# Optimization experiments

Hardware: AMD Instinct MI355X
Metric: run time of the kernel (lower is better)

The kernel has to match this reference:

```python
import jax, jax.numpy as jnp
import numpy as np

# ShiftedSteSign forward: binary sign (0 -> +1). STE only matters for backward.

def ste_sign(x):
    return jnp.where(x >= 0, 1.0, -1.0).astype(x.dtype)

N, D, U, E = 32768, 1024, 1024, 3  # tokens, d_in, units, kernel_estimators


def setup_inputs() -> dict:
    key = jax.random.key(0)
    kx, k0, k1, k2 = jax.random.split(key, 4)
    x = jax.random.normal(kx, (N, D), dtype=jnp.float32)
    # keras 'random_uniform' initializer default range [-0.05, 0.05]
    kernels = [jax.random.uniform(k, (D, U), jnp.float32, -0.05, 0.05) for k in (k0, k1, k2)]
    # alpha initialized as ||kernel||_1 along axis 0 divided by d_in (trainable)
    alphas = [jnp.sum(jnp.abs(kw), axis=0) / D for kw in kernels]
    return {"x": x,
            "k0": kernels[0], "k1": kernels[1], "k2": kernels[2],
            "a0": alphas[0], "a1": alphas[1], "a2": alphas[2]}


def reference(x, k0, k1, k2, a0, a1, a2):
    d = x.shape[-1]
    xq = ste_sign(x)                                   # [N, D] binary
    beta = jnp.sum(jnp.abs(x), axis=-1) / d            # [N]
    out = jnp.zeros((x.shape[0], k0.shape[1]), x.dtype)
    for kw, a in ((k0, a0), (k1, a1), (k2, a2)):
        Z = xq @ ste_sign(kw)                          # binary GEMM [N, U]
        out = out + Z * (beta[:, None] * a[None, :])   # outer-product scale
    return out
```

## Files before the change

kernel.cpp:

```cpp
#include <hip/hip_runtime.h>
#include <hip/hip_bf16.h>
#include <stdint.h>

#define N_TOK 32768
#define D_IN  1024
#define U_OUT 1024

typedef __attribute__((ext_vector_type(4))) int int32x4;

__device__ __forceinline__ void async_copy16(const void* g, void* l) {
  __builtin_amdgcn_global_load_lds(
      (const __attribute__((address_space(1))) void*)g,
      (__attribute__((address_space(3))) void*)l,
      16, 0, 0);
}

__global__ __launch_bounds__(256) void quant_kernel(
    const float* __restrict__ x,
    char* __restrict__ xq,
    float* __restrict__ beta) {
  const int wave = threadIdx.x >> 6;
  const int lane = threadIdx.x & 63;
  const int row  = blockIdx.x * 4 + wave;

  const float4* p = (const float4*)(x + (size_t)row * D_IN);
  alignas(16) char sb[16];
  float asum = 0.f;
  #pragma unroll
  for (int j = 0; j < 4; ++j) {
    const float4 v = p[lane * 4 + j];
    asum += fabsf(v.x) + fabsf(v.y) + fabsf(v.z) + fabsf(v.w);
    sb[j * 4 + 0] = (v.x >= 0.f) ? 1 : -1;
    sb[j * 4 + 1] = (v.y >= 0.f) ? 1 : -1;
    sb[j * 4 + 2] = (v.z >= 0.f) ? 1 : -1;
    sb[j * 4 + 3] = (v.w >= 0.f) ? 1 : -1;
  }
  *(int32x4*)(xq + (size_t)row * D_IN + lane * 16) = *(const int32x4*)sb;

  #pragma unroll
  for (int off = 32; off > 0; off >>= 1)
    asum += __shfl_down(asum, off, 64);
  if (lane == 0) beta[row] = asum * (1.0f / (float)D_IN);
}

__global__ __launch_bounds__(256) void wt_kernel(
    const float* __restrict__ k0, const float* __restrict__ k1,
    const float* __restrict__ k2,
    const float* __restrict__ a0, const float* __restrict__ a1,
    const float* __restrict__ a2,
    char* __restrict__ wt,
    float* __restrict__ q) {
  const int tid = threadIdx.x;
  const int d0  = blockIdx.x * 16;
  const int u0  = tid * 4;

  const float4 av0 = *(const float4*)(a0 + u0);
  const float4 av1 = *(const float4*)(a1 + u0);
  const float4 av2 = *(const float4*)(a2 + u0);
  float4 s;
  s.x = fmaxf(av0.x + av1.x + av2.x, 1e-20f);
  s.y = fmaxf(av0.y + av1.y + av2.y, 1e-20f);
  s.z = fmaxf(av0.z + av1.z + av2.z, 1e-20f);
  s.w = fmaxf(av0.w + av1.w + av2.w, 1e-20f);
  if (blockIdx.x == 0) {
    float4 qv;
    qv.x = s.x * (1.0f / 127.0f); qv.y = s.y * (1.0f / 127.0f);
    qv.z = s.z * (1.0f / 127.0f); qv.w = s.w * (1.0f / 127.0f);
    *(float4*)(q + u0) = qv;
  }
  const float4 inv = {127.0f / s.x, 127.0f / s.y, 127.0f / s.z, 127.0f / s.w};

  alignas(16) char buf[4][16];
  #pragma unroll
  for (int d = 0; d < 16; ++d) {
    const size_t off = (size_t)(d0 + d) * U_OUT + u0;
    const float4 v0 = *(const float4*)(k0 + off);
    const float4 v1 = *(const float4*)(k1 + off);
    const float4 v2 = *(const float4*)(k2 + off);
    float4 w;
    w.x = (v0.x >= 0.f ? av0.x : -av0.x) + (v1.x >= 0.f ? av1.x : -av1.x)
        + (v2.x >= 0.f ? av2.x : -av2.x);
    w.y = (v0.y >= 0.f ? av0.y : -av0.y) + (v1.y >= 0.f ? av1.y : -av1.y)
        + (v2.y >= 0.f ? av2.y : -av2.y);
    w.z = (v0.z >= 0.f ? av0.z : -av0.z) + (v1.z >= 0.f ? av1.z : -av1.z)
        + (v2.z >= 0.f ? av2.z : -av2.z);
    w.w = (v0.w >= 0.f ? av0.w : -av0.w) + (v1.w >= 0.f ? av1.w : -av1.w)
        + (v2.w >= 0.f ? av2.w : -av2.w);
    buf[0][d] = (char)(int)rintf(w.x * inv.x);
    buf[1][d] = (char)(int)rintf(w.y * inv.y);
    buf[2][d] = (char)(int)rintf(w.z * inv.z);
    buf[3][d] = (char)(int)rintf(w.w * inv.w);
  }
  #pragma unroll
  for (int j = 0; j < 4; ++j)
    *(int32x4*)(wt + (size_t)(u0 + j) * D_IN + d0) = *(const int32x4*)buf[j];
}

#define BM 128
#define BN 128
#define BK 64

__global__ __launch_bounds__(256, 2) void gemm_kernel(
    const char* __restrict__ A,
    const char* __restrict__ Bt,
    const float* __restrict__ beta,
    const float* __restrict__ q,
    float* __restrict__ C) {
  const int K = D_IN, N = U_OUT;
  __shared__ char As[BM * BK];
  __shared__ char Bs[BN * BK];

  const int bid = blockIdx.x;
  const int xcd = bid & 7;
  const int g   = bid >> 3;
  const int mt  = xcd * 32 + (g >> 3);
  const int nt  = g & 7;
  const int m0  = mt * BM;
  const int n0  = nt * BN;

  const int tid  = threadIdx.x;
  const int wave = tid >> 6;
  const int lane = tid & 63;
  const int wr   = wave >> 1;
  const int wc   = wave & 1;
  const int lrow = lane & 15;
  const int quad = lane >> 4;

  int32x4 acc[4][4] = {};

  for (int kk = 0; kk < K; kk += BK) {
    #pragma unroll
    for (int half = 0; half < 2; half++) {
      const int s   = tid + half * 256;
      const int row = s >> 2;
      const int c   = (s & 3) * 16;
      async_copy16(A  + (size_t)(m0 + row) * K + kk + c, As + (size_t)s * 16);
      async_copy16(Bt + (size_t)(n0 + row) * K + kk + c, Bs + (size_t)s * 16);
    }
    __syncthreads();

    int32x4 af[4], bf[4];
    #pragma unroll
    for (int i = 0; i < 4; i++) {
      af[i] = *(const int32x4*)(As + (wr * 64 + i * 16 + lrow) * BK + quad * 16);
      bf[i] = *(const int32x4*)(Bs + (wc * 64 + i * 16 + lrow) * BK + quad * 16);
    }
    #pragma unroll
    for (int mi = 0; mi < 4; mi++)
      #pragma unroll
      for (int ni = 0; ni < 4; ni++)
        acc[mi][ni] = __builtin_amdgcn_mfma_i32_16x16x64_i8(
            af[mi], bf[ni], acc[mi][ni], 0, 0, 0);
    __syncthreads();
  }

  #pragma unroll
  for (int mi = 0; mi < 4; mi++) {
    #pragma unroll
    for (int r = 0; r < 4; r++) {
      const int row = m0 + wr * 64 + mi * 16 + quad * 4 + r;
      const float b = beta[row];
      #pragma unroll
      for (int ni = 0; ni < 4; ni++) {
        const int col = n0 + wc * 64 + ni * 16 + lrow;
        C[(size_t)row * N + col] = (float)acc[mi][ni][r] * b * q[col];
      }
    }
  }
}

extern "C" void kernel_launch(void* const* d_in, const int* in_sizes, int n_in,
                              void* d_out, int out_size, void* d_ws, size_t ws_size,
                              hipStream_t stream) {
  const float* x  = (const float*)d_in[0];
  const float* k0 = (const float*)d_in[1];
  const float* k1 = (const float*)d_in[2];
  const float* k2 = (const float*)d_in[3];
  const float* a0 = (const float*)d_in[4];
  const float* a1 = (const float*)d_in[5];
  const float* a2 = (const float*)d_in[6];
  float* out = (float*)d_out;

  char* ws = (char*)d_ws;
  char*  xq   = ws;
  char*  wt   = ws + (size_t)N_TOK * D_IN;
  float* q    = (float*)(wt + (size_t)U_OUT * D_IN);
  float* beta = q + U_OUT;

  quant_kernel<<<N_TOK / 4, 256, 0, stream>>>(x, xq, beta);
  wt_kernel<<<64, 256, 0, stream>>>(k0, k1, k2, a0, a1, a2, wt, q);
  gemm_kernel<<<(N_TOK / BM) * (U_OUT / BN), 256, 0, stream>>>(xq, wt, beta, q, out);
}
```

Before: 289.7 us.

## Pipeline int8 GEMM with triple-buffered LDS, bigger tiles, and swizzled layout

The GEMM moves from 128x128 tiles with 256 threads to 256x256 tiles with 512 threads. A three-stage LDS ring prefetches the next K tiles with global_load_lds while MFMAs run, and an XOR swizzle is added to cut LDS bank conflicts. Each K step is split into two MFMA phases with barriers and s_setprio, q is hoisted into registers for the epilogue, and the quantize kernel switches to coalesced 4-byte stores. The costs are higher LDS and register use per block and hand-tuned vmcnt waits that must line up with the prefetch order.

Result: no change. 294.0 us (+1.5%).

```diff
diff --git a/kernel.cpp b/kernel.cpp
--- a/kernel.cpp
+++ b/kernel.cpp
@@ -1,5 +1,4 @@
 #include <hip/hip_runtime.h>
-#include <hip/hip_bf16.h>
 #include <stdint.h>
 
 #define N_TOK 32768
@@ -24,19 +23,18 @@
   const int row  = blockIdx.x * 4 + wave;
 
   const float4* p = (const float4*)(x + (size_t)row * D_IN);
-  alignas(16) char sb[16];
+  uint32_t* outw = (uint32_t*)(xq + (size_t)row * D_IN);
   float asum = 0.f;
   #pragma unroll
   for (int j = 0; j < 4; ++j) {
-    const float4 v = p[lane * 4 + j];
+    const float4 v = p[j * 64 + lane];
     asum += fabsf(v.x) + fabsf(v.y) + fabsf(v.z) + fabsf(v.w);
-    sb[j * 4 + 0] = (v.x >= 0.f) ? 1 : -1;
-    sb[j * 4 + 1] = (v.y >= 0.f) ? 1 : -1;
-    sb[j * 4 + 2] = (v.z >= 0.f) ? 1 : -1;
-    sb[j * 4 + 3] = (v.w >= 0.f) ? 1 : -1;
-  }
-  *(int32x4*)(xq + (size_t)row * D_IN + lane * 16) = *(const int32x4*)sb;
-
+    uint32_t w =  (uint32_t)(uint8_t)(char)(v.x >= 0.f ? 1 : -1)
+               | ((uint32_t)(uint8_t)(char)(v.y >= 0.f ? 1 : -1) << 8)
+               | ((uint32_t)(uint8_t)(char)(v.z >= 0.f ? 1 : -1) << 16)
+               | ((uint32_t)(uint8_t)(char)(v.w >= 0.f ? 1 : -1) << 24);
+    outw[j * 64 + lane] = w;
+  }
   #pragma unroll
   for (int off = 32; off > 0; off >>= 1)
     asum += __shfl_down(asum, off, 64);
@@ -96,74 +94,128 @@
     *(int32x4*)(wt + (size_t)(u0 + j) * D_IN + d0) = *(const int32x4*)buf[j];
 }
 
-#define BM 128
-#define BN 128
-#define BK 64
-
-__global__ __launch_bounds__(256, 2) void gemm_kernel(
+#define BM 256
+#define BN 256
+#define BKT 64
+#define NKT (D_IN / BKT)
+
+__global__ __launch_bounds__(512, 2) void gemm_kernel(
     const char* __restrict__ A,
     const char* __restrict__ Bt,
     const float* __restrict__ beta,
     const float* __restrict__ q,
     float* __restrict__ C) {
-  const int K = D_IN, N = U_OUT;
-  __shared__ char As[BM * BK];
-  __shared__ char Bs[BN * BK];
+  __shared__ char As[3][BM * BKT];
+  __shared__ char Bs[3][BN * BKT];
 
   const int bid = blockIdx.x;
   const int xcd = bid & 7;
   const int g   = bid >> 3;
-  const int mt  = xcd * 32 + (g >> 3);
-  const int nt  = g & 7;
-  const int m0  = mt * BM;
-  const int n0  = nt * BN;
+  const int m0  = (xcd * 16 + (g >> 2)) * BM;
+  const int n0  = (g & 3) * BN;
 
   const int tid  = threadIdx.x;
   const int wave = tid >> 6;
   const int lane = tid & 63;
-  const int wr   = wave >> 1;
-  const int wc   = wave & 1;
+  const int wr   = wave >> 2;
+  const int wc   = wave & 3;
   const int lrow = lane & 15;
   const int quad = lane >> 4;
 
-  int32x4 acc[4][4] = {};
-
-  for (int kk = 0; kk < K; kk += BK) {
-    #pragma unroll
-    for (int half = 0; half < 2; half++) {
-      const int s   = tid + half * 256;
-      const int row = s >> 2;
-      const int c   = (s & 3) * 16;
-      async_copy16(A  + (size_t)(m0 + row) * K + kk + c, As + (size_t)s * 16);
-      async_copy16(Bt + (size_t)(n0 + row) * K + kk + c, Bs + (size_t)s * 16);
-    }
-    __syncthreads();
+  const int srow = tid >> 2;
+  const int scol = (((tid & 3) ^ (srow & 3)) << 4);
+  const char* gA0 = A  + (size_t)(m0 +       srow) * D_IN + scol;
+  const char* gA1 = A  + (size_t)(m0 + 128 + srow) * D_IN + scol;
+  const char* gB0 = Bt + (size_t)(n0 +       srow) * D_IN + scol;
+  const char* gB1 = Bt + (size_t)(n0 + 128 + srow) * D_IN + scol;
+  const int ldst = tid * 16;
+
+  const int rdcol = ((quad ^ (lane & 3)) << 4);
+
+  int32x4 acc[8][4] = {};
+
+  async_copy16(gA0,        As[0] + ldst);
+  async_copy16(gA1,        As[0] + 8192 + ldst);
+  async_copy16(gB0,        Bs[0] + ldst);
+  async_copy16(gB1,        Bs[0] + 8192 + ldst);
+  async_copy16(gA0 + BKT,  As[1] + ldst);
+  async_copy16(gA1 + BKT,  As[1] + 8192 + ldst);
+  async_copy16(gB0 + BKT,  Bs[1] + ldst);
+  async_copy16(gB1 + BKT,  Bs[1] + 8192 + ldst);
+  asm volatile("s_waitcnt vmcnt(4)" ::: "memory");
+  __builtin_amdgcn_s_barrier();
+
+  int p = 0;
+  for (int T = 0; T < NKT; ++T) {
+    const char* Ap = As[p];
+    const char* Bp = Bs[p];
+    int pn = p + 2; if (pn >= 3) pn -= 3;
+    const bool st = (T + 2 < NKT);
+    const int kt2 = (T + 2) * BKT;
 
     int32x4 af[4], bf[4];
     #pragma unroll
-    for (int i = 0; i < 4; i++) {
-      af[i] = *(const int32x4*)(As + (wr * 64 + i * 16 + lrow) * BK + quad * 16);
-      bf[i] = *(const int32x4*)(Bs + (wc * 64 + i * 16 + lrow) * BK + quad * 16);
-    }
-    #pragma unroll
-    for (int mi = 0; mi < 4; mi++)
+    for (int i = 0; i < 4; ++i) {
+      af[i] = *(const int32x4*)(Ap + (wr * 128 + i * 16 + lrow) * BKT + rdcol);
+      bf[i] = *(const int32x4*)(Bp + (wc * 64  + i * 16 + lrow) * BKT + rdcol);
+    }
+    if (st) {
+      async_copy16(gA0 + kt2, As[pn] + ldst);
+      async_copy16(gA1 + kt2, As[pn] + 8192 + ldst);
+    }
+    __builtin_amdgcn_s_barrier();
+    __builtin_amdgcn_s_setprio(1);
+    #pragma unroll
+    for (int mi = 0; mi < 4; ++mi)
       #pragma unroll
-      for (int ni = 0; ni < 4; ni++)
+      for (int ni = 0; ni < 4; ++ni)
         acc[mi][ni] = __builtin_amdgcn_mfma_i32_16x16x64_i8(
             af[mi], bf[ni], acc[mi][ni], 0, 0, 0);
-    __syncthreads();
-  }
-
-  #pragma unroll
-  for (int mi = 0; mi < 4; mi++) {
-    #pragma unroll
-    for (int r = 0; r < 4; r++) {
-      const int row = m0 + wr * 64 + mi * 16 + quad * 4 + r;
+    __builtin_amdgcn_s_setprio(0);
+    __builtin_amdgcn_s_barrier();
+
+    int32x4 ag[4];
+    #pragma unroll
+    for (int i = 0; i < 4; ++i)
+      ag[i] = *(const int32x4*)(Ap + (wr * 128 + (i + 4) * 16 + lrow) * BKT + rdcol);
+    if (st) {
+      async_copy16(gB0 + kt2, Bs[pn] + ldst);
+      async_copy16(gB1 + kt2, Bs[pn] + 8192 + ldst);
+    }
+    __builtin_amdgcn_s_barrier();
+    __builtin_amdgcn_s_setprio(1);
+    #pragma unroll
+    for (int mi = 0; mi < 4; ++mi)
+      #pragma unroll
+      for (int ni = 0; ni < 4; ++ni)
+        acc[mi + 4][ni] = __builtin_amdgcn_mfma_i32_16x16x64_i8(
+            ag[mi], bf[ni], acc[mi + 4][ni], 0, 0, 0);
+    __builtin_amdgcn_s_setprio(0);
+
+    if (T < NKT - 2) {
+      asm volatile("s_waitcnt vmcnt(4)" ::: "memory");
+    } else if (T == NKT - 2) {
+      asm volatile("s_waitcnt vmcnt(0)" ::: "memory");
+    }
+    __builtin_amdgcn_s_barrier();
+
+    p = p + 1; if (p >= 3) p -= 3;
+  }
+
+  float qv[4];
+  #pragma unroll
+  for (int ni = 0; ni < 4; ++ni)
+    qv[ni] = q[n0 + wc * 64 + ni * 16 + lrow];
+  #pragma unroll
+  for (int mi = 0; mi < 8; ++mi) {
+    #pragma unroll
+    for (int r = 0; r < 4; ++r) {
+      const int row = m0 + wr * 128 + mi * 16 + quad * 4 + r;
       const float b = beta[row];
       #pragma unroll
-      for (int ni = 0; ni < 4; ni++) {
+      for (int ni = 0; ni < 4; ++ni) {
         const int col = n0 + wc * 64 + ni * 16 + lrow;
-        C[(size_t)row * N + col] = (float)acc[mi][ni][r] * b * q[col];
+        C[(size_t)row * U_OUT + col] = (float)acc[mi][ni][r] * b * qv[ni];
       }
     }
   }
@@ -189,5 +241,5 @@
 
   quant_kernel<<<N_TOK / 4, 256, 0, stream>>>(x, xq, beta);
   wt_kernel<<<64, 256, 0, stream>>>(k0, k1, k2, a0, a1, a2, wt, q);
-  gemm_kernel<<<(N_TOK / BM) * (U_OUT / BN), 256, 0, stream>>>(xq, wt, beta, q, out);
-}
+  gemm_kernel<<<(N_TOK / BM) * (U_OUT / BN), 512, 0, stream>>>(xq, wt, beta, q, out);
+}
```
